# Kernel tuning notes

Measured on AMD Instinct MI355X. Metric: run time of the kernel, lower is better.

Reference implementation:

```python
import jax, jax.numpy as jnp
import numpy as np

B, T, E, D = 32, 8192, 256, 32  # batch, seq, embed_dim, output_dim
H, M = D, 2 * D                 # SSM hidden_dim, mlp_dim


def _ssm_block(x, Win, bin_, log_a, Wout, bout, W1, b1, W2, b2):
    """Diagonal linear SSM scan + residual MLP. x: (B,T,D) -> (B,T,D)."""
    u = x @ Win + bin_                      # (B,T,H)
    a = jax.nn.sigmoid(log_a)               # (H,) per-channel decay in (0,1)
    aa = jnp.broadcast_to(a, u.shape)

    def comb(c1, c2):
        a1, h1 = c1
        a2, h2 = c2
        return a1 * a2, a2 * h1 + h2

    _, h = jax.lax.associative_scan(comb, (aa, u), axis=1)  # h_t = a*h_{t-1} + u_t
    y = h @ Wout + bout                      # (B,T,D)
    return y + jax.nn.gelu(y @ W1 + b1) @ W2 + b2


def setup_inputs() -> dict:
    key = jax.random.key(0)
    ks = jax.random.split(key, 20)
    s_in, s_d, s_m = 1.0 / np.sqrt(E), 1.0 / np.sqrt(D), 1.0 / np.sqrt(M)
    inp = {
        "e_seq": jax.random.normal(ks[0], (B, T, E), dtype=jnp.float32),
        "Wpi": jax.random.normal(ks[1], (E, D), dtype=jnp.float32) * s_in,
        "bpi": jnp.zeros((D,), jnp.float32),
        "Wpo": jax.random.normal(ks[2], (2 * D, D), dtype=jnp.float32) * s_d,
        "bpo": jnp.zeros((D,), jnp.float32),
    }
    for i, pfx in enumerate(["f", "b"]):
        o = 3 + 8 * i
        inp[pfx + "_Win"] = jax.random.normal(ks[o], (D, H), dtype=jnp.float32) * s_d
        inp[pfx + "_bin"] = jnp.zeros((H,), jnp.float32)
        inp[pfx + "_loga"] = jax.random.normal(ks[o + 1], (H,), dtype=jnp.float32)
        inp[pfx + "_Wout"] = jax.random.normal(ks[o + 2], (H, D), dtype=jnp.float32) * s_d
        inp[pfx + "_bout"] = jnp.zeros((D,), jnp.float32)
        inp[pfx + "_W1"] = jax.random.normal(ks[o + 3], (D, M), dtype=jnp.float32) * s_d
        inp[pfx + "_b1"] = jnp.zeros((M,), jnp.float32)
        inp[pfx + "_W2"] = jax.random.normal(ks[o + 4], (M, D), dtype=jnp.float32) * s_m
        inp[pfx + "_b2"] = jnp.zeros((D,), jnp.float32)
    return inp


def reference(e_seq, Wpi, bpi, Wpo, bpo,
              f_Win, f_bin, f_loga, f_Wout, f_bout, f_W1, f_b1, f_W2, f_b2,
              b_Win, b_bin, b_loga, b_Wout, b_bout, b_W1, b_b1, b_W2, b_b2):
    x = e_seq @ Wpi + bpi                                    # (B,T,D)
    fwd = _ssm_block(x, f_Win, f_bin, f_loga, f_Wout, f_bout, f_W1, f_b1, f_W2, f_b2)
    bwd = _ssm_block(x[:, ::-1], b_Win, b_bin, b_loga, b_Wout, b_bout,
                     b_W1, b_b1, b_W2, b_b2)[:, ::-1]
    combined = jnp.concatenate([fwd, bwd], axis=-1)           # (B,T,2D)
    return combined @ Wpo + bpo                               # (B,T,D)
```

## Files before the change

kernel.cpp:

```cpp
#include <hip/hip_runtime.h>


typedef unsigned short u16;
typedef unsigned int   u32;
typedef __bf16 bf16x8 __attribute__((ext_vector_type(8)));
typedef float  f32x4  __attribute__((ext_vector_type(4)));

constexpr int BB = 32, TT = 8192, NCH = 64;
constexpr int BT = BB * TT;
constexpr int LCH = 256;
constexpr int NCHUNK = TT / LCH;

#define MFMA16(av, bv, cc) __builtin_amdgcn_mfma_f32_16x16x32_bf16((av), (bv), (cc), 0, 0, 0)

__device__ __forceinline__ u16 f2bf(float x) {
    union { float f; u32 u; } v; v.f = x;
    u32 r = (v.u + 0x7FFFu + ((v.u >> 16) & 1u)) >> 16;
    return (u16)r;
}
__device__ __forceinline__ float bf2f(u16 x) {
    union { u32 u; float f; } v; v.u = ((u32)x) << 16;
    return v.f;
}
__device__ __forceinline__ float gelu_tanh(float x) {
    float inner = 0.7978845608028654f * fmaf(0.044715f * x, x * x, x);
    float ez = __expf(2.f * inner);
    float t = 1.f - 2.f / (ez + 1.f);
    return 0.5f * x * (1.f + t);
}

__global__ void k0_prep(const float* __restrict__ Wpi, const float* __restrict__ bpi,
                        const float* __restrict__ fWin, const float* __restrict__ fbin,
                        const float* __restrict__ floga,
                        const float* __restrict__ bWin, const float* __restrict__ bbin,
                        const float* __restrict__ bloga,
                        const float* __restrict__ fW1, const float* __restrict__ bW1,
                        const float* __restrict__ fW2, const float* __restrict__ bW2,
                        const float* __restrict__ fb2, const float* __restrict__ bb2,
                        const float* __restrict__ fWout, const float* __restrict__ bWout,
                        const float* __restrict__ Wpo, const float* __restrict__ bpo,
                        u16* __restrict__ WuT, float* __restrict__ bu,
                        float* __restrict__ a_arr, float* __restrict__ l2a,
                        u16* __restrict__ W1Tbf, u16* __restrict__ W2poCatT,
                        u16* __restrict__ WoutTbf, u16* __restrict__ WpoCatT,
                        float* __restrict__ bc)
{
    const int blk = blockIdx.x, tid = threadIdx.x;
    if (blk < 64) {
        const float* Win = (blk < 32) ? fWin : bWin;
        const int nn = blk & 31;
        float s = 0.f;
        #pragma unroll
        for (int d = 0; d < 32; ++d) s = fmaf(Wpi[tid * 32 + d], Win[d * 32 + nn], s);
        WuT[blk * 256 + tid] = f2bf(s);
        if (tid == 0) {
            const float* bin = (blk < 32) ? fbin : bbin;
            float sb = bin[nn];
            for (int d = 0; d < 32; ++d) sb = fmaf(bpi[d], Win[d * 32 + nn], sb);
            bu[blk] = sb;
        }
    } else if (blk == 64) {
        if (tid < 64) {
            const float* lg = (tid < 32) ? floga : bloga;
            float a = 1.f / (1.f + __expf(-lg[tid & 31]));
            a_arr[tid] = a;
            l2a[tid] = log2f(a);
        } else if (tid < 96) {
            int i = tid - 64;
            float s = bpo[i];
            for (int d = 0; d < 32; ++d) s = fmaf(fb2[d], Wpo[d * 32 + i], s);
            for (int d = 0; d < 32; ++d) s = fmaf(bb2[d], Wpo[(32 + d) * 32 + i], s);
            bc[i] = s;
        }
    } else if (blk == 65 || blk == 66) {
        int dir = blk - 65;
        const float* W1 = dir ? bW1 : fW1;
        for (int x = tid; x < 2048; x += 256) {
            int n = x >> 5, k = x & 31;
            W1Tbf[dir * 2048 + n * 32 + k] = f2bf(W1[k * 64 + n]);
        }
    } else if (blk == 67 || blk == 68) {
        int dir = blk - 67;
        const float* W2 = dir ? bW2 : fW2;
        const float* Wp = Wpo + dir * 32 * 32;
        for (int x = tid; x < 2048; x += 256) {
            int j = x >> 5, i = x & 31;
            float s = 0.f;
            for (int d = 0; d < 32; ++d) s = fmaf(W2[j * 32 + d], Wp[d * 32 + i], s);
            W2poCatT[i * 128 + dir * 64 + j] = f2bf(s);
        }
    } else if (blk == 69 || blk == 70) {
        int dir = blk - 69;
        const float* Wout = dir ? bWout : fWout;
        for (int x = tid; x < 1024; x += 256) {
            int n = x >> 5, k = x & 31;
            WoutTbf[dir * 1024 + n * 32 + k] = f2bf(Wout[k * 32 + n]);
        }
    } else {
        for (int x = tid; x < 2048; x += 256) {
            int n = x >> 6, k = x & 63;
            WpoCatT[n * 64 + k] = f2bf(Wpo[k * 32 + n]);
        }
    }
}

__global__ __launch_bounds__(256) void kA_proj_scan(const float* __restrict__ e,
    const u16* __restrict__ WuT, const float* __restrict__ bu,
    const float* __restrict__ a_arr, const float* __restrict__ l2a,
    u16* __restrict__ h, float* __restrict__ Ebuf)
{
    __shared__ __align__(16) u16 As[32][264];
    __shared__ __align__(16) u16 utile[256 * 64];
    __shared__ float eSub[64][4];
    const int tid = threadIdx.x;
    const int blk = blockIdx.x;
    const size_t t0 = (size_t)blk * 256;
    const int lane = tid & 63, wave = tid >> 6;
    const int row16 = lane & 15, quad = lane >> 4;
    const int wr = (wave & 1) * 16;
    const int wc = (wave >> 1) * 32;

    #pragma unroll 1
    for (int s = 0; s < 8; ++s) {
        const float4* eg = reinterpret_cast<const float4*>(e + (t0 + s * 32) * 256);
        #pragma unroll
        for (int it = 0; it < 8; ++it) {
            int i = tid + it * 256;
            int r = i >> 6, kk = (i & 63) << 2;
            float4 v = eg[i];
            uint2 pk;
            pk.x = (u32)f2bf(v.x) | ((u32)f2bf(v.y) << 16);
            pk.y = (u32)f2bf(v.z) | ((u32)f2bf(v.w) << 16);
            *reinterpret_cast<uint2*>(&As[r][kk]) = pk;
        }
        __syncthreads();
        f32x4 acc[2] = {{0.f,0.f,0.f,0.f},{0.f,0.f,0.f,0.f}};
        #pragma unroll
        for (int ks = 0; ks < 8; ++ks) {
            bf16x8 av = *reinterpret_cast<const bf16x8*>(&As[wr + row16][ks * 32 + quad * 8]);
            #pragma unroll
            for (int c2 = 0; c2 < 2; ++c2) {
                bf16x8 bv = *reinterpret_cast<const bf16x8*>(WuT + (wc + c2 * 16 + row16) * 256 + ks * 32 + quad * 8);
                acc[c2] = MFMA16(av, bv, acc[c2]);
            }
        }
        #pragma unroll
        for (int c2 = 0; c2 < 2; ++c2) {
            int col = wc + c2 * 16 + row16;
            float bias = bu[col];
            #pragma unroll
            for (int r = 0; r < 4; ++r) {
                int trow = s * 32 + wr + quad * 4 + r;
                utile[trow * 64 + col] = f2bf(acc[c2][r] + bias);
            }
        }
        __syncthreads();
    }

    const int ch = tid & 63, sid = tid >> 6;
    const float a = a_arr[ch];
    const bool fwd = (ch < 32);
    float hh = 0.f;
    if (fwd) {
        for (int i = 0; i < 64; ++i) { int t = sid * 64 + i;
            hh = fmaf(a, hh, bf2f(utile[t * 64 + ch])); utile[t * 64 + ch] = f2bf(hh); }
    } else {
        for (int i = 63; i >= 0; --i) { int t = sid * 64 + i;
            hh = fmaf(a, hh, bf2f(utile[t * 64 + ch])); utile[t * 64 + ch] = f2bf(hh); }
    }
    eSub[ch][sid] = hh;
    __syncthreads();
    const float A = exp2f(64.f * l2a[ch]);
    float cin = 0.f;
    if (fwd) { for (int j = 0; j < sid; ++j) cin = fmaf(A, cin, eSub[ch][j]); }
    else     { for (int j = 3; j > sid; --j) cin = fmaf(A, cin, eSub[ch][j]); }
    if (fwd && sid == 3)  Ebuf[(size_t)blk * 64 + ch] = fmaf(A, cin, eSub[ch][3]);
    if (!fwd && sid == 0) Ebuf[(size_t)blk * 64 + ch] = fmaf(A, cin, eSub[ch][0]);
    float p = cin;
    if (fwd) {
        for (int i = 0; i < 64; ++i) { int t = sid * 64 + i; p *= a;
            utile[t * 64 + ch] = f2bf(bf2f(utile[t * 64 + ch]) + p); }
    } else {
        for (int i = 63; i >= 0; --i) { int t = sid * 64 + i; p *= a;
            utile[t * 64 + ch] = f2bf(bf2f(utile[t * 64 + ch]) + p); }
    }
    __syncthreads();
    uint4* gw = reinterpret_cast<uint4*>(h + t0 * 64);
    const uint4* s4 = reinterpret_cast<const uint4*>(utile);
    #pragma unroll
    for (int i = 0; i < 8; ++i) gw[tid + 256 * i] = s4[tid + 256 * i];
}

__global__ void k3_carry(const float* __restrict__ Ebuf, float* __restrict__ Cin,
                         const float* __restrict__ l2a)
{
    int tid = blockIdx.x * 256 + threadIdx.x;
    if (tid >= BB * NCH) return;
    int b = tid >> 6, ch = tid & 63;
    float aL = exp2f((float)LCH * l2a[ch]);
    float S = 0.f;
    if (ch < 32) {
        for (int c = 0; c < NCHUNK; ++c) {
            size_t idx = ((size_t)(b * NCHUNK + c)) * 64 + ch;
            Cin[idx] = S; S = fmaf(aL, S, Ebuf[idx]);
        }
    } else {
        for (int c = NCHUNK - 1; c >= 0; --c) {
            size_t idx = ((size_t)(b * NCHUNK + c)) * 64 + ch;
            Cin[idx] = S; S = fmaf(aL, S, Ebuf[idx]);
        }
    }
}

__global__ __launch_bounds__(256) void kB_out(const u16* __restrict__ h,
    const float* __restrict__ Cin, const float* __restrict__ l2a,
    const u16* __restrict__ WoutTbf, const float* __restrict__ fbout, const float* __restrict__ bbout,
    const u16* __restrict__ W1Tbf, const float* __restrict__ fb1, const float* __restrict__ bb1,
    const u16* __restrict__ WpoCatT, const u16* __restrict__ W2poCatT,
    const float* __restrict__ bc, float* __restrict__ out)
{
    __shared__ __align__(16) u16 Yt[256 * 64];
    __shared__ __align__(16) u16 Zw[4][16 * 128];
    const int tid = threadIdx.x;
    const int blk = blockIdx.x;
    const size_t t0 = (size_t)blk * 256;
    const int lane = tid & 63, wave = tid >> 6;
    const int row16 = lane & 15, quad = lane >> 4;
    const float* cinp = Cin + (size_t)blk * 64;

    #pragma unroll 1
    for (int rr = 0; rr < 4; ++rr) {
        const int rt = wave * 4 + rr;
        const int kpos = rt * 16 + row16;
        #pragma unroll
        for (int dir = 0; dir < 2; ++dir) {
            uint4 hv = *reinterpret_cast<const uint4*>(h + (t0 + kpos) * 64 + dir * 32 + quad * 8);
            u32 hw[4] = {hv.x, hv.y, hv.z, hv.w};
            const float off = dir ? (float)(LCH - kpos) : (float)(kpos + 1);
            union { bf16x8 v; u16 s[8]; } af;
            #pragma unroll
            for (int j = 0; j < 8; ++j) {
                int chn = dir * 32 + quad * 8 + j;
                float f = bf2f((u16)((hw[j >> 1] >> ((j & 1) * 16)) & 0xFFFFu));
                f = fmaf(cinp[chn], exp2f(off * l2a[chn]), f);
                af.s[j] = f2bf(f);
            }
            f32x4 yv[2] = {{0.f,0.f,0.f,0.f},{0.f,0.f,0.f,0.f}};
            #pragma unroll
            for (int nt = 0; nt < 2; ++nt) {
                bf16x8 bv = *reinterpret_cast<const bf16x8*>(WoutTbf + dir * 1024 + (nt * 16 + row16) * 32 + quad * 8);
                yv[nt] = MFMA16(af.v, bv, yv[nt]);
            }
            const float* boutp = dir ? bbout : fbout;
            #pragma unroll
            for (int nt = 0; nt < 2; ++nt) {
                float bb = boutp[nt * 16 + row16];
                #pragma unroll
                for (int r = 0; r < 4; ++r) {
                    int row = rt * 16 + quad * 4 + r;
                    int col = dir * 32 + nt * 16 + row16;
                    int cs = (col >> 3) ^ (row & 7);
                    Yt[row * 64 + cs * 8 + (col & 7)] = f2bf(yv[nt][r] + bb);
                }
            }
        }
    }

    #pragma unroll 1
    for (int rr = 0; rr < 4; ++rr) {
        const int rt = wave * 4 + rr;
        const int arow = rt * 16 + row16;
        f32x4 o0 = {0.f,0.f,0.f,0.f}, o1 = {0.f,0.f,0.f,0.f};

        #pragma unroll
        for (int kb = 0; kb < 2; ++kb) {
            int cs = (kb * 4 + quad) ^ (arow & 7);
            bf16x8 av = *reinterpret_cast<const bf16x8*>(&Yt[arow * 64 + cs * 8]);
            bf16x8 bv0 = *reinterpret_cast<const bf16x8*>(WpoCatT + (row16) * 64 + kb * 32 + quad * 8);
            bf16x8 bv1 = *reinterpret_cast<const bf16x8*>(WpoCatT + (16 + row16) * 64 + kb * 32 + quad * 8);
            o0 = MFMA16(av, bv0, o0);
            o1 = MFMA16(av, bv1, o1);
        }
        #pragma unroll
        for (int dir = 0; dir < 2; ++dir) {
            int cs = (dir * 4 + quad) ^ (arow & 7);
            bf16x8 av = *reinterpret_cast<const bf16x8*>(&Yt[arow * 64 + cs * 8]);
            const float* b1p = dir ? bb1 : fb1;
            #pragma unroll
            for (int nt2 = 0; nt2 < 4; ++nt2) {
                f32x4 z = {0.f,0.f,0.f,0.f};
                bf16x8 bv = *reinterpret_cast<const bf16x8*>(W1Tbf + dir * 2048 + (nt2 * 16 + row16) * 32 + quad * 8);
                z = MFMA16(av, bv, z);
                float bb = b1p[nt2 * 16 + row16];
                #pragma unroll
                for (int r = 0; r < 4; ++r) {
                    float zz = gelu_tanh(z[r] + bb);
                    int zrow = quad * 4 + r;
                    int zcol = dir * 64 + nt2 * 16 + row16;
                    int zcs = (zcol >> 3) ^ (zrow & 7);
                    Zw[wave][zrow * 128 + zcs * 8 + (zcol & 7)] = f2bf(zz);
                }
            }
        }
        #pragma unroll
        for (int kb = 0; kb < 4; ++kb) {
            int zcs = (kb * 4 + quad) ^ (row16 & 7);
            bf16x8 av = *reinterpret_cast<const bf16x8*>(&Zw[wave][row16 * 128 + zcs * 8]);
            bf16x8 bv0 = *reinterpret_cast<const bf16x8*>(W2poCatT + (row16) * 128 + kb * 32 + quad * 8);
            bf16x8 bv1 = *reinterpret_cast<const bf16x8*>(W2poCatT + (16 + row16) * 128 + kb * 32 + quad * 8);
            o0 = MFMA16(av, bv0, o0);
            o1 = MFMA16(av, bv1, o1);
        }
        #pragma unroll
        for (int r = 0; r < 4; ++r) {
            size_t row = t0 + rt * 16 + quad * 4 + r;
            out[row * 32 + row16]      = o0[r] + bc[row16];
            out[row * 32 + 16 + row16] = o1[r] + bc[16 + row16];
        }
    }
}

extern "C" void kernel_launch(void* const* d_in, const int* in_sizes, int n_in,
                              void* d_out, int out_size, void* d_ws, size_t ws_size,
                              hipStream_t stream)
{
    (void)in_sizes; (void)n_in; (void)out_size; (void)ws_size;
    const float* e     = (const float*)d_in[0];
    const float* Wpi   = (const float*)d_in[1];
    const float* bpi   = (const float*)d_in[2];
    const float* Wpo   = (const float*)d_in[3];
    const float* bpo   = (const float*)d_in[4];
    const float* fWin  = (const float*)d_in[5];
    const float* fbin  = (const float*)d_in[6];
    const float* floga = (const float*)d_in[7];
    const float* fWout = (const float*)d_in[8];
    const float* fbout = (const float*)d_in[9];
    const float* fW1   = (const float*)d_in[10];
    const float* fb1   = (const float*)d_in[11];
    const float* fW2   = (const float*)d_in[12];
    const float* fb2   = (const float*)d_in[13];
    const float* bWin  = (const float*)d_in[14];
    const float* bbin  = (const float*)d_in[15];
    const float* bloga = (const float*)d_in[16];
    const float* bWout = (const float*)d_in[17];
    const float* bbout = (const float*)d_in[18];
    const float* bW1   = (const float*)d_in[19];
    const float* bb1   = (const float*)d_in[20];
    const float* bW2   = (const float*)d_in[21];
    const float* bb2   = (const float*)d_in[22];
    float* outp = (float*)d_out;

    char* ws = (char*)d_ws;
    size_t off = 0;
    auto walloc = [&](size_t bytes) { void* p = ws + off; off += (bytes + 255) & ~(size_t)255; return p; };
    u16*   hbuf  = (u16*)  walloc((size_t)BT * 64 * 2);
    u16*   WuT   = (u16*)  walloc(64 * 256 * 2);
    float* bu    = (float*)walloc(64 * 4);
    float* a_arr = (float*)walloc(64 * 4);
    float* l2a   = (float*)walloc(64 * 4);
    float* Ebuf  = (float*)walloc((size_t)BB * NCHUNK * 64 * 4);
    float* Cin   = (float*)walloc((size_t)BB * NCHUNK * 64 * 4);
    u16*   W1Tbf    = (u16*)walloc(2 * 64 * 32 * 2);
    u16*   W2poCatT = (u16*)walloc(32 * 128 * 2);
    u16*   WoutTbf  = (u16*)walloc(2 * 32 * 32 * 2);
    u16*   WpoCatT  = (u16*)walloc(32 * 64 * 2);
    float* bc    = (float*)walloc(32 * 4);

    k0_prep<<<72, 256, 0, stream>>>(Wpi, bpi, fWin, fbin, floga, bWin, bbin, bloga,
                                    fW1, bW1, fW2, bW2, fb2, bb2, fWout, bWout, Wpo, bpo,
                                    WuT, bu, a_arr, l2a, W1Tbf, W2poCatT, WoutTbf, WpoCatT, bc);
    kA_proj_scan<<<BB * NCHUNK, 256, 0, stream>>>(e, WuT, bu, a_arr, l2a, hbuf, Ebuf);
    k3_carry<<<8, 256, 0, stream>>>(Ebuf, Cin, l2a);
    kB_out<<<BB * NCHUNK, 256, 0, stream>>>(hbuf, Cin, l2a,
                                            WoutTbf, fbout, bbout,
                                            W1Tbf, fb1, bb1,
                                            WpoCatT, W2poCatT, bc, outp);
}
```

Baseline: 467.6 us.

## Load projection inputs directly into registers, widen scan block, fuse output stages

```diff
diff --git a/kernel.cpp b/kernel.cpp
--- a/kernel.cpp
+++ b/kernel.cpp
@@ -104,91 +104,95 @@
     }
 }
 
-__global__ __launch_bounds__(256) void kA_proj_scan(const float* __restrict__ e,
+__global__ __launch_bounds__(512, 4) void kA_proj_scan(const float* __restrict__ e,
     const u16* __restrict__ WuT, const float* __restrict__ bu,
     const float* __restrict__ a_arr, const float* __restrict__ l2a,
     u16* __restrict__ h, float* __restrict__ Ebuf)
 {
-    __shared__ __align__(16) u16 As[32][264];
     __shared__ __align__(16) u16 utile[256 * 64];
-    __shared__ float eSub[64][4];
+    __shared__ float eSub[64][8];
     const int tid = threadIdx.x;
     const int blk = blockIdx.x;
     const size_t t0 = (size_t)blk * 256;
     const int lane = tid & 63, wave = tid >> 6;
     const int row16 = lane & 15, quad = lane >> 4;
-    const int wr = (wave & 1) * 16;
-    const int wc = (wave >> 1) * 32;
-
-    #pragma unroll 1
-    for (int s = 0; s < 8; ++s) {
-        const float4* eg = reinterpret_cast<const float4*>(e + (t0 + s * 32) * 256);
-        #pragma unroll
-        for (int it = 0; it < 8; ++it) {
-            int i = tid + it * 256;
-            int r = i >> 6, kk = (i & 63) << 2;
-            float4 v = eg[i];
-            uint2 pk;
-            pk.x = (u32)f2bf(v.x) | ((u32)f2bf(v.y) << 16);
-            pk.y = (u32)f2bf(v.z) | ((u32)f2bf(v.w) << 16);
-            *reinterpret_cast<uint2*>(&As[r][kk]) = pk;
-        }
-        __syncthreads();
-        f32x4 acc[2] = {{0.f,0.f,0.f,0.f},{0.f,0.f,0.f,0.f}};
-        #pragma unroll
-        for (int ks = 0; ks < 8; ++ks) {
-            bf16x8 av = *reinterpret_cast<const bf16x8*>(&As[wr + row16][ks * 32 + quad * 8]);
-            #pragma unroll
-            for (int c2 = 0; c2 < 2; ++c2) {
-                bf16x8 bv = *reinterpret_cast<const bf16x8*>(WuT + (wc + c2 * 16 + row16) * 256 + ks * 32 + quad * 8);
-                acc[c2] = MFMA16(av, bv, acc[c2]);
-            }
-        }
-        #pragma unroll
-        for (int c2 = 0; c2 < 2; ++c2) {
-            int col = wc + c2 * 16 + row16;
+
+    f32x4 acc[2][4];
+    #pragma unroll
+    for (int rt = 0; rt < 2; ++rt)
+        #pragma unroll
+        for (int nt = 0; nt < 4; ++nt) acc[rt][nt] = f32x4{0.f, 0.f, 0.f, 0.f};
+
+    const float* eBase = e + (t0 + wave * 32 + row16) * 256;
+
+    #pragma unroll 2
+    for (int ks = 0; ks < 8; ++ks) {
+        bf16x8 bv[4];
+        #pragma unroll
+        for (int nt = 0; nt < 4; ++nt)
+            bv[nt] = *reinterpret_cast<const bf16x8*>(WuT + (nt * 16 + row16) * 256 + ks * 32 + quad * 8);
+        #pragma unroll
+        for (int rt = 0; rt < 2; ++rt) {
+            const float* ep = eBase + rt * 16 * 256 + ks * 32 + quad * 8;
+            float4 v0 = *reinterpret_cast<const float4*>(ep);
+            float4 v1 = *reinterpret_cast<const float4*>(ep + 4);
+            union { bf16x8 v; u16 s[8]; } af;
+            af.s[0] = f2bf(v0.x); af.s[1] = f2bf(v0.y);
+            af.s[2] = f2bf(v0.z); af.s[3] = f2bf(v0.w);
+            af.s[4] = f2bf(v1.x); af.s[5] = f2bf(v1.y);
+            af.s[6] = f2bf(v1.z); af.s[7] = f2bf(v1.w);
+            #pragma unroll
+            for (int nt = 0; nt < 4; ++nt)
+                acc[rt][nt] = MFMA16(af.v, bv[nt], acc[rt][nt]);
+        }
+    }
+    #pragma unroll
+    for (int rt = 0; rt < 2; ++rt) {
+        #pragma unroll
+        for (int nt = 0; nt < 4; ++nt) {
+            int col = nt * 16 + row16;
             float bias = bu[col];
             #pragma unroll
             for (int r = 0; r < 4; ++r) {
-                int trow = s * 32 + wr + quad * 4 + r;
-                utile[trow * 64 + col] = f2bf(acc[c2][r] + bias);
-            }
-        }
-        __syncthreads();
-    }
+                int trow = wave * 32 + rt * 16 + quad * 4 + r;
+                utile[trow * 64 + col] = f2bf(acc[rt][nt][r] + bias);
+            }
+        }
+    }
+    __syncthreads();
 
     const int ch = tid & 63, sid = tid >> 6;
     const float a = a_arr[ch];
     const bool fwd = (ch < 32);
     float hh = 0.f;
     if (fwd) {
-        for (int i = 0; i < 64; ++i) { int t = sid * 64 + i;
+        for (int i = 0; i < 32; ++i) { int t = sid * 32 + i;
             hh = fmaf(a, hh, bf2f(utile[t * 64 + ch])); utile[t * 64 + ch] = f2bf(hh); }
     } else {
-        for (int i = 63; i >= 0; --i) { int t = sid * 64 + i;
+        for (int i = 31; i >= 0; --i) { int t = sid * 32 + i;
             hh = fmaf(a, hh, bf2f(utile[t * 64 + ch])); utile[t * 64 + ch] = f2bf(hh); }
     }
     eSub[ch][sid] = hh;
     __syncthreads();
-    const float A = exp2f(64.f * l2a[ch]);
+    const float A = exp2f(32.f * l2a[ch]);
     float cin = 0.f;
     if (fwd) { for (int j = 0; j < sid; ++j) cin = fmaf(A, cin, eSub[ch][j]); }
-    else     { for (int j = 3; j > sid; --j) cin = fmaf(A, cin, eSub[ch][j]); }
-    if (fwd && sid == 3)  Ebuf[(size_t)blk * 64 + ch] = fmaf(A, cin, eSub[ch][3]);
+    else     { for (int j = 7; j > sid; --j) cin = fmaf(A, cin, eSub[ch][j]); }
+    if (fwd && sid == 7)  Ebuf[(size_t)blk * 64 + ch] = fmaf(A, cin, eSub[ch][7]);
     if (!fwd && sid == 0) Ebuf[(size_t)blk * 64 + ch] = fmaf(A, cin, eSub[ch][0]);
     float p = cin;
     if (fwd) {
-        for (int i = 0; i < 64; ++i) { int t = sid * 64 + i; p *= a;
+        for (int i = 0; i < 32; ++i) { int t = sid * 32 + i; p *= a;
             utile[t * 64 + ch] = f2bf(bf2f(utile[t * 64 + ch]) + p); }
     } else {
-        for (int i = 63; i >= 0; --i) { int t = sid * 64 + i; p *= a;
+        for (int i = 31; i >= 0; --i) { int t = sid * 32 + i; p *= a;
             utile[t * 64 + ch] = f2bf(bf2f(utile[t * 64 + ch]) + p); }
     }
     __syncthreads();
     uint4* gw = reinterpret_cast<uint4*>(h + t0 * 64);
     const uint4* s4 = reinterpret_cast<const uint4*>(utile);
     #pragma unroll
-    for (int i = 0; i < 8; ++i) gw[tid + 256 * i] = s4[tid + 256 * i];
+    for (int i = 0; i < 4; ++i) gw[tid + 512 * i] = s4[tid + 512 * i];
 }
 
 __global__ void k3_carry(const float* __restrict__ Ebuf, float* __restrict__ Cin,
@@ -198,28 +202,32 @@
     if (tid >= BB * NCH) return;
     int b = tid >> 6, ch = tid & 63;
     float aL = exp2f((float)LCH * l2a[ch]);
+    const size_t base = (size_t)b * NCHUNK * 64 + ch;
+    float ev[NCHUNK];
+    #pragma unroll
+    for (int c = 0; c < NCHUNK; ++c) ev[c] = Ebuf[base + (size_t)c * 64];
     float S = 0.f;
     if (ch < 32) {
+        #pragma unroll
         for (int c = 0; c < NCHUNK; ++c) {
-            size_t idx = ((size_t)(b * NCHUNK + c)) * 64 + ch;
-            Cin[idx] = S; S = fmaf(aL, S, Ebuf[idx]);
+            Cin[base + (size_t)c * 64] = S; S = fmaf(aL, S, ev[c]);
         }
     } else {
+        #pragma unroll
         for (int c = NCHUNK - 1; c >= 0; --c) {
-            size_t idx = ((size_t)(b * NCHUNK + c)) * 64 + ch;
-            Cin[idx] = S; S = fmaf(aL, S, Ebuf[idx]);
-        }
-    }
-}
-
-__global__ __launch_bounds__(256) void kB_out(const u16* __restrict__ h,
+            Cin[base + (size_t)c * 64] = S; S = fmaf(aL, S, ev[c]);
+        }
+    }
+}
+
+__global__ __launch_bounds__(256, 4) void kB_out(const u16* __restrict__ h,
     const float* __restrict__ Cin, const float* __restrict__ l2a,
     const u16* __restrict__ WoutTbf, const float* __restrict__ fbout, const float* __restrict__ bbout,
     const u16* __restrict__ W1Tbf, const float* __restrict__ fb1, const float* __restrict__ bb1,
     const u16* __restrict__ WpoCatT, const u16* __restrict__ W2poCatT,
     const float* __restrict__ bc, float* __restrict__ out)
 {
-    __shared__ __align__(16) u16 Yt[256 * 64];
+    __shared__ __align__(16) u16 Yt[4][16 * 64];
     __shared__ __align__(16) u16 Zw[4][16 * 128];
     const int tid = threadIdx.x;
     const int blk = blockIdx.x;
@@ -227,11 +235,14 @@
     const int lane = tid & 63, wave = tid >> 6;
     const int row16 = lane & 15, quad = lane >> 4;
     const float* cinp = Cin + (size_t)blk * 64;
+    u16* myY = Yt[wave];
+    u16* myZ = Zw[wave];
 
     #pragma unroll 1
     for (int rr = 0; rr < 4; ++rr) {
         const int rt = wave * 4 + rr;
         const int kpos = rt * 16 + row16;
+
         #pragma unroll
         for (int dir = 0; dir < 2; ++dir) {
             uint4 hv = *reinterpret_cast<const uint4*>(h + (t0 + kpos) * 64 + dir * 32 + quad * 8);
@@ -257,25 +268,20 @@
                 float bb = boutp[nt * 16 + row16];
                 #pragma unroll
                 for (int r = 0; r < 4; ++r) {
-                    int row = rt * 16 + quad * 4 + r;
+                    int row = quad * 4 + r;
                     int col = dir * 32 + nt * 16 + row16;
                     int cs = (col >> 3) ^ (row & 7);
-                    Yt[row * 64 + cs * 8 + (col & 7)] = f2bf(yv[nt][r] + bb);
+                    myY[row * 64 + cs * 8 + (col & 7)] = f2bf(yv[nt][r] + bb);
                 }
             }
         }
-    }
-
-    #pragma unroll 1
-    for (int rr = 0; rr < 4; ++rr) {
-        const int rt = wave * 4 + rr;
-        const int arow = rt * 16 + row16;
+
         f32x4 o0 = {0.f,0.f,0.f,0.f}, o1 = {0.f,0.f,0.f,0.f};
 
         #pragma unroll
         for (int kb = 0; kb < 2; ++kb) {
-            int cs = (kb * 4 + quad) ^ (arow & 7);
-            bf16x8 av = *reinterpret_cast<const bf16x8*>(&Yt[arow * 64 + cs * 8]);
+            int cs = (kb * 4 + quad) ^ (row16 & 7);
+            bf16x8 av = *reinterpret_cast<const bf16x8*>(&myY[row16 * 64 + cs * 8]);
             bf16x8 bv0 = *reinterpret_cast<const bf16x8*>(WpoCatT + (row16) * 64 + kb * 32 + quad * 8);
             bf16x8 bv1 = *reinterpret_cast<const bf16x8*>(WpoCatT + (16 + row16) * 64 + kb * 32 + quad * 8);
             o0 = MFMA16(av, bv0, o0);
@@ -283,8 +289,8 @@
         }
         #pragma unroll
         for (int dir = 0; dir < 2; ++dir) {
-            int cs = (dir * 4 + quad) ^ (arow & 7);
-            bf16x8 av = *reinterpret_cast<const bf16x8*>(&Yt[arow * 64 + cs * 8]);
+            int cs = (dir * 4 + quad) ^ (row16 & 7);
+            bf16x8 av = *reinterpret_cast<const bf16x8*>(&myY[row16 * 64 + cs * 8]);
             const float* b1p = dir ? bb1 : fb1;
             #pragma unroll
             for (int nt2 = 0; nt2 < 4; ++nt2) {
@@ -298,14 +304,14 @@
                     int zrow = quad * 4 + r;
                     int zcol = dir * 64 + nt2 * 16 + row16;
                     int zcs = (zcol >> 3) ^ (zrow & 7);
-                    Zw[wave][zrow * 128 + zcs * 8 + (zcol & 7)] = f2bf(zz);
+                    myZ[zrow * 128 + zcs * 8 + (zcol & 7)] = f2bf(zz);
                 }
             }
         }
         #pragma unroll
         for (int kb = 0; kb < 4; ++kb) {
             int zcs = (kb * 4 + quad) ^ (row16 & 7);
-            bf16x8 av = *reinterpret_cast<const bf16x8*>(&Zw[wave][row16 * 128 + zcs * 8]);
+            bf16x8 av = *reinterpret_cast<const bf16x8*>(&myZ[row16 * 128 + zcs * 8]);
             bf16x8 bv0 = *reinterpret_cast<const bf16x8*>(W2poCatT + (row16) * 128 + kb * 32 + quad * 8);
             bf16x8 bv1 = *reinterpret_cast<const bf16x8*>(W2poCatT + (16 + row16) * 128 + kb * 32 + quad * 8);
             o0 = MFMA16(av, bv0, o0);
@@ -369,7 +375,7 @@
     k0_prep<<<72, 256, 0, stream>>>(Wpi, bpi, fWin, fbin, floga, bWin, bbin, bloga,
                                     fW1, bW1, fW2, bW2, fb2, bb2, fWout, bWout, Wpo, bpo,
                                     WuT, bu, a_arr, l2a, W1Tbf, W2poCatT, WoutTbf, WpoCatT, bc);
-    kA_proj_scan<<<BB * NCHUNK, 256, 0, stream>>>(e, WuT, bu, a_arr, l2a, hbuf, Ebuf);
+    kA_proj_scan<<<BB * NCHUNK, 512, 0, stream>>>(e, WuT, bu, a_arr, l2a, hbuf, Ebuf);
     k3_carry<<<8, 256, 0, stream>>>(Ebuf, Cin, l2a);
     kB_out<<<BB * NCHUNK, 256, 0, stream>>>(hbuf, Cin, l2a,
                                             WoutTbf, fbout, bbout,
```

New measurement: 535.4 us. 14.5% more time.
